# Optimization experiments

Hardware: AMD Instinct MI355X
Metric: run time of the kernel (lower is better)

## Reference

```python
import jax, jax.numpy as jnp
import numpy as np

N, E = 50000, 500000
IN_C, HID, OUT_C, HEADS, NL = 128, 16, 16, 8, 4
EPS = 1e-5
NEG_SLOPE = 0.2


def _gatv2(x, src, dst, Wl, Wr, att, bias, concat):
    # GATv2Conv (PyG semantics, eval mode): lin_l on source, lin_r on target,
    # e = a . LeakyReLU(xl[src] + xr[dst]); segment softmax over dst; scatter-sum.
    n = x.shape[0]
    H, C = att.shape
    xl = (x @ Wl).reshape(n, H, C)
    xr = (x @ Wr).reshape(n, H, C)
    e = jax.nn.leaky_relu(xl[src] + xr[dst], NEG_SLOPE)          # [E', H, C]
    logit = jnp.einsum('ehc,hc->eh', e, att)                      # [E', H]
    mx = jax.lax.stop_gradient(jax.ops.segment_max(logit, dst, num_segments=n))
    a = jnp.exp(logit - mx[dst])
    denom = jax.ops.segment_sum(a, dst, num_segments=n)
    alpha = a / denom[dst]                                        # [E', H]
    out = jax.ops.segment_sum(xl[src] * alpha[..., None], dst, num_segments=n)
    out = out.reshape(n, H * C) if concat else out.mean(axis=1)
    return out + bias


def _bn_eval(x, g, b, m, v):
    return (x - m) * jax.lax.rsqrt(v + EPS) * g + b


def setup_inputs() -> dict:
    key = jax.random.key(0)
    ks = jax.random.split(key, 32)
    d = {}
    d['x'] = jax.random.normal(ks[0], (N, IN_C), dtype=jnp.float32)
    d['edge_index'] = jax.random.randint(ks[1], (2, E), 0, N, dtype=jnp.int64)
    HC = HID * HEADS  # 128
    dims_in = [IN_C, HC, HC, HC]
    dims_h = [HEADS, HEADS, HEADS, 1]
    dims_c = [HID, HID, HID, OUT_C]
    ki = 2
    for i in range(NL):
        fan = dims_in[i]
        s = 1.0 / np.sqrt(fan)
        d[f'W{i}l'] = jax.random.uniform(ks[ki], (fan, dims_h[i] * dims_c[i]), minval=-s, maxval=s, dtype=jnp.float32); ki += 1
        d[f'W{i}r'] = jax.random.uniform(ks[ki], (fan, dims_h[i] * dims_c[i]), minval=-s, maxval=s, dtype=jnp.float32); ki += 1
        d[f'a{i}'] = jax.random.normal(ks[ki], (dims_h[i], dims_c[i]), dtype=jnp.float32) * 0.1; ki += 1
        out_dim = dims_h[i] * dims_c[i] if i < NL - 1 else dims_c[i]
        d[f'b{i}'] = jnp.zeros((out_dim,), dtype=jnp.float32)
    for i in range(NL - 1):
        d[f'g{i}'] = jnp.ones((HC,), dtype=jnp.float32) + 0.1 * jax.random.normal(ks[ki], (HC,), dtype=jnp.float32); ki += 1
        d[f'be{i}'] = 0.1 * jax.random.normal(ks[ki], (HC,), dtype=jnp.float32); ki += 1
        d[f'm{i}'] = 0.1 * jax.random.normal(ks[ki], (HC,), dtype=jnp.float32); ki += 1
        d[f'v{i}'] = jnp.ones((HC,), dtype=jnp.float32)
    return d


def reference(x, edge_index, W0l, W0r, a0, b0, W1l, W1r, a1, b1, W2l, W2r, a2, b2, W3l, W3r, a3, b3, g0, be0, m0, v0, g1, be1, m1, v1, g2, be2, m2, v2):
    n = x.shape[0]
    loop = jnp.arange(n, dtype=edge_index.dtype)
    src = jnp.concatenate([edge_index[0], loop])  # add_self_loops=True (PyG default)
    dst = jnp.concatenate([edge_index[1], loop])
    Ws = [(W0l, W0r, a0, b0), (W1l, W1r, a1, b1), (W2l, W2r, a2, b2), (W3l, W3r, a3, b3)]
    bns = [(g0, be0, m0, v0), (g1, be1, m1, v1), (g2, be2, m2, v2)]
    h = x
    for i in range(NL):
        Wl, Wr, att, bias = Ws[i]
        h = _gatv2(h, src, dst, Wl, Wr, att, bias, concat=(i < NL - 1))
        if i < NL - 1:
            g, b, m, v = bns[i]
            h = jax.nn.elu(_bn_eval(h, g, b, m, v))
    return h
```

## Files before the change

### kernel.cpp

```cpp
#include <hip/hip_runtime.h>
#include <hip/hip_fp16.h>
#include <math.h>

static constexpr float BN_EPS = 1e-5f;
static constexpr float NEG = 0.2f;

typedef float f32x4 __attribute__((ext_vector_type(4)));
typedef _Float16 h16x2 __attribute__((ext_vector_type(2)));
typedef _Float16 h16x8 __attribute__((ext_vector_type(8)));


__global__ __launch_bounds__(256) void hist_pack(
    const int* __restrict__ ei, int E, int n, int* __restrict__ cnt,
    const float* __restrict__ W0l, const float* __restrict__ W0r,
    const float* __restrict__ W1l, const float* __restrict__ W1r,
    const float* __restrict__ W2l, const float* __restrict__ W2r,
    const float* __restrict__ W3l, const float* __restrict__ W3r,
    __half* __restrict__ pk0, __half* __restrict__ pk1,
    __half* __restrict__ pk2, __half* __restrict__ pk3) {
    int b = blockIdx.x;
    if (b < 200) {
        if (threadIdx.x >= 64) return;
        const float *Wl, *Wr;
        __half* packed;
        int tile, NTT, M;
        if (b < 192) {
            int layer = b >> 6;
            tile = b & 63;
            NTT = 16; M = 128;
            Wl = (layer == 0) ? W0l : (layer == 1) ? W1l : W2l;
            Wr = (layer == 0) ? W0r : (layer == 1) ? W1r : W2r;
            packed = (layer == 0) ? pk0 : (layer == 1) ? pk1 : pk2;
        } else {
            tile = b - 192;
            NTT = 2; M = 16;
            Wl = W3l; Wr = W3r; packed = pk3;
        }
        int NT = NTT >> 1;
        int gnt = tile % NTT;
        int kt = tile / NTT;
        int l = threadIdx.x;
        const float* W = (gnt < NT) ? Wl : Wr;
        int col = (gnt % NT) * 16 + (l & 15);
        int krow = kt * 32 + ((l >> 4) << 3);
        size_t base = (size_t)tile * 512 + (size_t)l * 8;
#pragma unroll
        for (int j = 0; j < 8; j++)
            packed[base + j] = __float2half(W[(size_t)(krow + j) * M + col]);
    } else {
        int e = (b - 200) * 256 + threadIdx.x;
        int ET = E + n;
        if (e >= ET) return;
        int d = (e < E) ? ei[E + e] : (e - E);
        atomicAdd(&cnt[d], 1);
    }
}


__global__ void scan_block(const int* __restrict__ cnt, int* __restrict__ rowptr,
                           int* __restrict__ bsums, int n) {
    __shared__ int s[1024];
    int i = blockIdx.x * 1024 + threadIdx.x;
    int vv = (i < n) ? cnt[i] : 0;
    s[threadIdx.x] = vv;
    __syncthreads();
    for (int d = 1; d < 1024; d <<= 1) {
        int t = (threadIdx.x >= d) ? s[threadIdx.x - d] : 0;
        __syncthreads();
        s[threadIdx.x] += t;
        __syncthreads();
    }
    if (i < n) rowptr[i + 1] = s[threadIdx.x];
    if (threadIdx.x == 1023) bsums[blockIdx.x] = s[1023];
}

__global__ void scan_bsums(int* __restrict__ bsums, int nb) {
    int L = threadIdx.x;
    int v = (L < nb) ? bsums[L] : 0;
    for (int d = 1; d < 64; d <<= 1) {
        int t = __shfl_up(v, d);
        if (L >= d) v += t;
    }
    int ex = __shfl_up(v, 1);
    if (L == 0) ex = 0;
    if (L < nb) bsums[L] = ex;
}

__global__ void scan_add(int* __restrict__ rowptr, const int* __restrict__ bsums, int n) {
    int i = blockIdx.x * 1024 + threadIdx.x;
    if (i < n) rowptr[i + 1] += bsums[blockIdx.x];
    if (i == 0) rowptr[0] = 0;
}

__global__ void scatter_kernel(const int* __restrict__ ei, int E, int n,
                               const int* __restrict__ rowptr, int* __restrict__ fill,
                               int* __restrict__ col) {
    int e = blockIdx.x * blockDim.x + threadIdx.x;
    int ET = E + n;
    if (e >= ET) return;
    int s, d;
    if (e < E) { s = ei[e]; d = ei[E + e]; } else { s = e - E; d = s; }
    int pos = atomicAdd(&fill[d], 1);
    col[rowptr[d] + pos] = s;
}


template <bool FIRST>
__global__ __launch_bounds__(256) void gemm_h_big(
    const __half* __restrict__ xh, const float* __restrict__ xf,
    const __half* __restrict__ packed,
    __half* __restrict__ Y1, __half* __restrict__ Y2, int n) {
    __shared__ _Float16 sA[64 * 136];
    const int t = threadIdx.x;
    const int row0 = blockIdx.x * 64;

    for (int c = t; c < 1024; c += 256) {
        int row = c >> 4;
        int off = (c & 15) * 8;
        int gr = row0 + row;
        if (gr >= n) gr = n - 1;
        if (FIRST) {
            float4 v0 = *(const float4*)&xf[(size_t)gr * 128 + off];
            float4 v1 = *(const float4*)&xf[(size_t)gr * 128 + off + 4];
            h16x8 h = {(_Float16)v0.x, (_Float16)v0.y, (_Float16)v0.z, (_Float16)v0.w,
                       (_Float16)v1.x, (_Float16)v1.y, (_Float16)v1.z, (_Float16)v1.w};
            *(h16x8*)&sA[row * 136 + off] = h;
        } else {
            *(h16x8*)&sA[row * 136 + off] = *(const h16x8*)&xh[(size_t)gr * 128 + off];
        }
    }
    __syncthreads();

    const int lane = t & 63;
    const int s = t >> 6;
    const int lr = lane & 15;
    const int kq = (lane >> 4) * 8;

    h16x8 af[4][4];
#pragma unroll
    for (int rt = 0; rt < 4; rt++)
#pragma unroll
        for (int kt = 0; kt < 4; kt++)
            af[rt][kt] = *(const h16x8*)&sA[(rt * 16 + lr) * 136 + kt * 32 + kq];

    f32x4 acc[4][4];
#pragma unroll
    for (int a = 0; a < 4; a++)
#pragma unroll
        for (int b = 0; b < 4; b++) acc[a][b] = (f32x4){0.f, 0.f, 0.f, 0.f};

#pragma unroll
    for (int kt = 0; kt < 4; kt++) {
#pragma unroll
        for (int ntl = 0; ntl < 4; ntl++) {
            int nt = s * 4 + ntl;
            h16x8 b = *(const h16x8*)&packed[((size_t)(kt * 16 + nt)) * 512 + lane * 8];
#pragma unroll
            for (int rt = 0; rt < 4; rt++)
                acc[ntl][rt] = __builtin_amdgcn_mfma_f32_16x16x32_f16(af[rt][kt], b, acc[ntl][rt], 0, 0, 0);
        }
    }

    __half* Y = (s < 2) ? Y1 : Y2;
    const int colh = (s & 1) * 64;
    const int rq = (lane >> 4) * 4;
#pragma unroll
    for (int ntl = 0; ntl < 4; ntl++) {
        int col = colh + ntl * 16 + lr;
#pragma unroll
        for (int rt = 0; rt < 4; rt++) {
#pragma unroll
            for (int g = 0; g < 4; g++) {
                int row = row0 + rt * 16 + rq + g;
                if (row < n) Y[(size_t)row * 128 + col] = __float2half(acc[ntl][rt][g]);
            }
        }
    }
}


__global__ __launch_bounds__(256) void gemm_h_small(
    const __half* __restrict__ xh, const __half* __restrict__ packed,
    float* __restrict__ Y1, float* __restrict__ Y2, int n) {
    int lane = threadIdx.x & 63;
    int wv = blockIdx.x * 4 + (threadIdx.x >> 6);
    int row0 = wv * 16;
    if (row0 >= n) return;
    int r = row0 + (lane & 15);
    if (r >= n) r = n - 1;
    int kq = (lane >> 4) * 8;

    h16x8 af[4];
#pragma unroll
    for (int kt = 0; kt < 4; kt++)
        af[kt] = *(const h16x8*)&xh[(size_t)r * 128 + kt * 32 + kq];

    f32x4 acc[2];
    acc[0] = (f32x4){0.f, 0.f, 0.f, 0.f};
    acc[1] = (f32x4){0.f, 0.f, 0.f, 0.f};

#pragma unroll
    for (int kt = 0; kt < 4; kt++) {
#pragma unroll
        for (int nt = 0; nt < 2; nt++) {
            h16x8 b = *(const h16x8*)&packed[((size_t)(kt * 2 + nt)) * 512 + lane * 8];
            acc[nt] = __builtin_amdgcn_mfma_f32_16x16x32_f16(af[kt], b, acc[nt], 0, 0, 0);
        }
    }

    int colb = lane & 15;
    int rbase = row0 + (lane >> 4) * 4;
#pragma unroll
    for (int nt = 0; nt < 2; nt++) {
        float* Y = (nt == 0) ? Y1 : Y2;
#pragma unroll
        for (int g = 0; g < 4; g++) {
            int row = rbase + g;
            if (row < n) Y[(size_t)row * 16 + colb] = acc[nt][g];
        }
    }
}


__device__ __forceinline__ float dot4_h(h16x2 l01, h16x2 l23,
                                        h16x2 a01, h16x2 a23) {
#if __has_builtin(__builtin_amdgcn_fdot2)
    float part = __builtin_amdgcn_fdot2(l01, a01, 0.f, false);
    return __builtin_amdgcn_fdot2(l23, a23, part, false);
#else
    return fmaf((float)l01.x, (float)a01.x, fmaf((float)l01.y, (float)a01.y,
           fmaf((float)l23.x, (float)a23.x, (float)l23.y * (float)a23.y)));
#endif
}

__global__ __launch_bounds__(256) void agg_h(
    const __half* __restrict__ xl, const __half* __restrict__ xr,
    const int* __restrict__ rowptr, const int* __restrict__ col,
    const float* __restrict__ att, const float* __restrict__ bias,
    const float* __restrict__ g, const float* __restrict__ be,
    const float* __restrict__ bm, const float* __restrict__ bv,
    __half* __restrict__ oh, int n) {
    int v = (blockIdx.x * blockDim.x + threadIdx.x) >> 6;
    if (v >= n) return;
    int lane = threadIdx.x & 63;
    int half = lane >> 5;
    int L = lane & 31;
    int ch = 4 * L;

    float2 rraw = *(const float2*)&xr[(size_t)v * 128 + ch];
    h16x2 rx01 = *(h16x2*)&rraw.x;
    h16x2 rx23 = *(h16x2*)&rraw.y;
    float4 av = *(const float4*)&att[ch];
    h16x2 a01 = {(_Float16)av.x, (_Float16)av.y};
    h16x2 a23 = {(_Float16)av.z, (_Float16)av.w};
    const h16x2 neg2 = {(_Float16)NEG, (_Float16)NEG};

    int beg = rowptr[v];
    int end = rowptr[v + 1];

    float lrun = 0.f;
    float4 acc = make_float4(0.f, 0.f, 0.f, 0.f);

    auto proc = [&](float2 raw, bool ok) {
        h16x2 h01 = *(h16x2*)&raw.x;
        h16x2 h23 = *(h16x2*)&raw.y;
        h16x2 s01 = h01 + rx01;
        h16x2 s23 = h23 + rx23;
        h16x2 l01 = __builtin_elementwise_max(s01, s01 * neg2);
        h16x2 l23 = __builtin_elementwise_max(s23, s23 * neg2);
        float part = dot4_h(l01, l23, a01, a23);
        part += __shfl_xor(part, 1);
        part += __shfl_xor(part, 2);
        float p = ok ? __expf(part) : 0.f;
        lrun += p;
        acc.x = fmaf(p, (float)h01.x, acc.x);
        acc.y = fmaf(p, (float)h01.y, acc.y);
        acc.z = fmaf(p, (float)h23.x, acc.z);
        acc.w = fmaf(p, (float)h23.y, acc.w);
    };

    int e = beg;
    for (; e + 8 <= end; e += 8) {
        float2 r[4];
#pragma unroll
        for (int j = 0; j < 4; j++) {
            int u = col[e + 2 * j + half];
            r[j] = *(const float2*)&xl[((size_t)u << 7) + ch];
        }
#pragma unroll
        for (int j = 0; j < 4; j++) proc(r[j], true);
    }
    for (; e < end; e += 4) {
        float2 r[2];
        bool ok[2];
#pragma unroll
        for (int j = 0; j < 2; j++) {
            int idx = e + 2 * j + half;
            ok[j] = (idx < end);
            r[j] = make_float2(0.f, 0.f);
            if (ok[j]) {
                int u = col[idx];
                r[j] = *(const float2*)&xl[((size_t)u << 7) + ch];
            }
        }
#pragma unroll
        for (int j = 0; j < 2; j++) proc(r[j], ok[j]);
    }

    lrun += __shfl_xor(lrun, 32);
    acc.x += __shfl_xor(acc.x, 32);
    acc.y += __shfl_xor(acc.y, 32);
    acc.z += __shfl_xor(acc.z, 32);
    acc.w += __shfl_xor(acc.w, 32);

    if (half == 0) {
        float inv = 1.0f / lrun;
        float4 b4 = *(const float4*)&bias[ch];
        float o[4] = {fmaf(acc.x, inv, b4.x), fmaf(acc.y, inv, b4.y),
                      fmaf(acc.z, inv, b4.z), fmaf(acc.w, inv, b4.w)};
        float4 m4 = *(const float4*)&bm[ch];
        float4 v4 = *(const float4*)&bv[ch];
        float4 g4 = *(const float4*)&g[ch];
        float4 e4 = *(const float4*)&be[ch];
        float ms[4] = {m4.x, m4.y, m4.z, m4.w};
        float vs[4] = {v4.x, v4.y, v4.z, v4.w};
        float gs[4] = {g4.x, g4.y, g4.z, g4.w};
        float es[4] = {e4.x, e4.y, e4.z, e4.w};
        unsigned short h[4];
#pragma unroll
        for (int j = 0; j < 4; j++) {
            o[j] = (o[j] - ms[j]) * rsqrtf(vs[j] + BN_EPS) * gs[j] + es[j];
            o[j] = o[j] > 0.f ? o[j] : expm1f(o[j]);
            h[j] = __half_as_ushort(__float2half(o[j]));
        }
        *(ushort4*)&oh[(size_t)v * 128 + ch] = make_ushort4(h[0], h[1], h[2], h[3]);
    }
}


__global__ __launch_bounds__(256) void agg_f(
    const float* __restrict__ xl, const float* __restrict__ xr,
    const int* __restrict__ rowptr, const int* __restrict__ col,
    const float* __restrict__ att, const float* __restrict__ bias,
    float* __restrict__ out, int n) {
    int v = (blockIdx.x * blockDim.x + threadIdx.x) >> 6;
    if (v >= n) return;
    int lane = threadIdx.x & 63;
    int slot = lane >> 2;
    int L = lane & 3;
    int ch = 4 * L;

    float4 xrv = *(const float4*)&xr[(size_t)v * 16 + ch];
    float4 av = *(const float4*)&att[ch];
    int beg = rowptr[v];
    int end = rowptr[v + 1];

    float lrun = 0.f;
    float4 acc = make_float4(0.f, 0.f, 0.f, 0.f);

    for (int eb = beg; eb < end; eb += 16) {
        int idx = eb + slot;
        bool ok = (idx < end);
        float4 xv = make_float4(0.f, 0.f, 0.f, 0.f);
        if (ok) {
            int u = col[idx];
            xv = *(const float4*)&xl[((size_t)u << 4) + ch];
        }
        float s0 = xv.x + xrv.x; s0 = s0 > 0.f ? s0 : NEG * s0;
        float s1 = xv.y + xrv.y; s1 = s1 > 0.f ? s1 : NEG * s1;
        float s2 = xv.z + xrv.z; s2 = s2 > 0.f ? s2 : NEG * s2;
        float s3 = xv.w + xrv.w; s3 = s3 > 0.f ? s3 : NEG * s3;
        float part = fmaf(s0, av.x, fmaf(s1, av.y, fmaf(s2, av.z, s3 * av.w)));
        part += __shfl_xor(part, 1);
        part += __shfl_xor(part, 2);
        float p = ok ? __expf(part) : 0.f;
        lrun += p;
        acc.x = fmaf(p, xv.x, acc.x);
        acc.y = fmaf(p, xv.y, acc.y);
        acc.z = fmaf(p, xv.z, acc.z);
        acc.w = fmaf(p, xv.w, acc.w);
    }

#pragma unroll
    for (int d = 4; d < 64; d <<= 1) {
        lrun += __shfl_xor(lrun, d);
        acc.x += __shfl_xor(acc.x, d);
        acc.y += __shfl_xor(acc.y, d);
        acc.z += __shfl_xor(acc.z, d);
        acc.w += __shfl_xor(acc.w, d);
    }

    if (slot == 0) {
        float inv = 1.0f / lrun;
        float4 b4 = *(const float4*)&bias[ch];
        *(float4*)&out[(size_t)v * 16 + ch] =
            make_float4(fmaf(acc.x, inv, b4.x), fmaf(acc.y, inv, b4.y),
                        fmaf(acc.z, inv, b4.z), fmaf(acc.w, inv, b4.w));
    }
}


extern "C" void kernel_launch(void* const* d_in, const int* in_sizes, int n_in,
                              void* d_out, int out_size, void* d_ws, size_t ws_size,
                              hipStream_t stream) {
    const float* x = (const float*)d_in[0];
    const int* ei = (const int*)d_in[1];
    const float* Wl[4] = {(const float*)d_in[2], (const float*)d_in[6],
                          (const float*)d_in[10], (const float*)d_in[14]};
    const float* Wr[4] = {(const float*)d_in[3], (const float*)d_in[7],
                          (const float*)d_in[11], (const float*)d_in[15]};
    const float* att[4] = {(const float*)d_in[4], (const float*)d_in[8],
                           (const float*)d_in[12], (const float*)d_in[16]};
    const float* bias[4] = {(const float*)d_in[5], (const float*)d_in[9],
                            (const float*)d_in[13], (const float*)d_in[17]};
    const float* g[3] = {(const float*)d_in[18], (const float*)d_in[22], (const float*)d_in[26]};
    const float* be[3] = {(const float*)d_in[19], (const float*)d_in[23], (const float*)d_in[27]};
    const float* bm[3] = {(const float*)d_in[20], (const float*)d_in[24], (const float*)d_in[28]};
    const float* bv[3] = {(const float*)d_in[21], (const float*)d_in[25], (const float*)d_in[29]};

    const int n = in_sizes[0] / 128;
    const int E = in_sizes[1] / 2;
    const int ET = E + n;

    char* p = (char*)d_ws;
    __half* xh = (__half*)p;           p += (size_t)n * 128 * 2;
    __half* xlh = (__half*)p;          p += (size_t)n * 128 * 2;
    __half* xrh = (__half*)p;          p += (size_t)n * 128 * 2;
    float* xl3 = (float*)p;            p += (size_t)n * 16 * 4;
    float* xr3 = (float*)p;            p += (size_t)n * 16 * 4;
    int* rowptr = (int*)p;            p += (size_t)(n + 1) * 4;
    int* cnt = (int*)p;               p += (size_t)n * 4;
    int* fill = (int*)p;              p += (size_t)n * 4;
    int* col = (int*)p;               p += (size_t)ET * 4;
    int* bsums = (int*)p;             p += 256;
    __half* pk[4];
    for (int i = 0; i < 3; i++) { pk[i] = (__half*)p; p += 4 * 16 * 512 * 2; }
    pk[3] = (__half*)p;               p += 4 * 2 * 512 * 2;

    (void)hipMemsetAsync(cnt, 0, (size_t)n * 8, stream);

    const int tb = 256;
    const int histBlocks = (ET + tb - 1) / tb;
    hist_pack<<<200 + histBlocks, tb, 0, stream>>>(
        ei, E, n, cnt,
        Wl[0], Wr[0], Wl[1], Wr[1], Wl[2], Wr[2], Wl[3], Wr[3],
        pk[0], pk[1], pk[2], pk[3]);
    int nb = (n + 1023) / 1024;
    scan_block<<<nb, 1024, 0, stream>>>(cnt, rowptr, bsums, n);
    scan_bsums<<<1, 64, 0, stream>>>(bsums, nb);
    scan_add<<<nb, 1024, 0, stream>>>(rowptr, bsums, n);
    scatter_kernel<<<(ET + tb - 1) / tb, tb, 0, stream>>>(ei, E, n, rowptr, fill, col);

    const int gb64 = (n + 63) / 64;
    const int gemmBlocksSmall = ((n + 15) / 16 + 3) / 4;
    const int aggBlocks = (n + 3) / 4;

    gemm_h_big<true><<<gb64, 256, 0, stream>>>(nullptr, x, pk[0], xlh, xrh, n);
    agg_h<<<aggBlocks, 256, 0, stream>>>(
        xlh, xrh, rowptr, col, att[0], bias[0], g[0], be[0], bm[0], bv[0], xh, n);
    for (int i = 1; i < 3; i++) {
        gemm_h_big<false><<<gb64, 256, 0, stream>>>(xh, nullptr, pk[i], xlh, xrh, n);
        agg_h<<<aggBlocks, 256, 0, stream>>>(
            xlh, xrh, rowptr, col, att[i], bias[i], g[i], be[i], bm[i], bv[i], xh, n);
    }
    gemm_h_small<<<gemmBlocksSmall, 256, 0, stream>>>(xh, pk[3], xl3, xr3, n);
    agg_f<<<aggBlocks, 256, 0, stream>>>(
        xl3, xr3, rowptr, col, att[3], bias[3], (float*)d_out, n);
}
```

Baseline: 363.6 us.

## Fuse scan with first GEMM, merge scan kernels, widen aggregation to 8-channel lanes

The block scan now runs in the same launch as the layer-0 GEMM, and the bsums scan is folded into the scan-add kernel, removing two launches. The half-precision aggregation is reorganised so each lane handles 8 channels with 16-byte loads and processes 4 edges per wave step. Neighbour indices are loaded once per 64-edge chunk and broadcast with shuffles instead of re-read per edge. The float aggregation uses the same shuffle-broadcast of indices. The cost is more registers per lane and added shuffle traffic.

```diff
diff --git a/kernel.cpp b/kernel.cpp
--- a/kernel.cpp
+++ b/kernel.cpp
@@ -57,38 +57,56 @@
 }
 
 
-__global__ void scan_block(const int* __restrict__ cnt, int* __restrict__ rowptr,
-                           int* __restrict__ bsums, int n) {
-    __shared__ int s[1024];
+__device__ __forceinline__ void scan_block_body256(
+    const int* __restrict__ cnt, int* __restrict__ rowptr,
+    int* __restrict__ bsums, int n, int bid, int* s) {
+    int t = threadIdx.x;
+    int base = bid * 1024 + t * 4;
+    int v0 = 0, v1 = 0, v2 = 0, v3 = 0;
+    if (base + 3 < n) {
+        v0 = cnt[base];     v1 = cnt[base + 1];
+        v2 = cnt[base + 2]; v3 = cnt[base + 3];
+    } else {
+        if (base < n)     v0 = cnt[base];
+        if (base + 1 < n) v1 = cnt[base + 1];
+        if (base + 2 < n) v2 = cnt[base + 2];
+        if (base + 3 < n) v3 = cnt[base + 3];
+    }
+    int p1 = v0 + v1, p2 = p1 + v2, p3 = p2 + v3;
+    s[t] = p3;
+    __syncthreads();
+    for (int d = 1; d < 256; d <<= 1) {
+        int tt = (t >= d) ? s[t - d] : 0;
+        __syncthreads();
+        s[t] += tt;
+        __syncthreads();
+    }
+    int ex = s[t] - p3;
+    if (base < n)     rowptr[base + 1] = ex + v0;
+    if (base + 1 < n) rowptr[base + 2] = ex + p1;
+    if (base + 2 < n) rowptr[base + 3] = ex + p2;
+    if (base + 3 < n) rowptr[base + 4] = ex + p3;
+    if (t == 255) bsums[bid] = s[255];
+}
+
+__global__ __launch_bounds__(1024) void scan_add2(
+    int* __restrict__ rowptr, const int* __restrict__ bsums, int n, int nb) {
+    __shared__ int sex;
+    if (threadIdx.x < 64) {
+        int L = threadIdx.x;
+        int v = (L < nb) ? bsums[L] : 0;
+#pragma unroll
+        for (int d = 1; d < 64; d <<= 1) {
+            int t = __shfl_up(v, d);
+            if (L >= d) v += t;
+        }
+        int ex = __shfl_up(v, 1);
+        if (L == 0) ex = 0;
+        if (L == (int)blockIdx.x) sex = ex;
+    }
+    __syncthreads();
     int i = blockIdx.x * 1024 + threadIdx.x;
-    int vv = (i < n) ? cnt[i] : 0;
-    s[threadIdx.x] = vv;
-    __syncthreads();
-    for (int d = 1; d < 1024; d <<= 1) {
-        int t = (threadIdx.x >= d) ? s[threadIdx.x - d] : 0;
-        __syncthreads();
-        s[threadIdx.x] += t;
-        __syncthreads();
-    }
-    if (i < n) rowptr[i + 1] = s[threadIdx.x];
-    if (threadIdx.x == 1023) bsums[blockIdx.x] = s[1023];
-}
-
-__global__ void scan_bsums(int* __restrict__ bsums, int nb) {
-    int L = threadIdx.x;
-    int v = (L < nb) ? bsums[L] : 0;
-    for (int d = 1; d < 64; d <<= 1) {
-        int t = __shfl_up(v, d);
-        if (L >= d) v += t;
-    }
-    int ex = __shfl_up(v, 1);
-    if (L == 0) ex = 0;
-    if (L < nb) bsums[L] = ex;
-}
-
-__global__ void scan_add(int* __restrict__ rowptr, const int* __restrict__ bsums, int n) {
-    int i = blockIdx.x * 1024 + threadIdx.x;
-    if (i < n) rowptr[i + 1] += bsums[blockIdx.x];
+    if (i < n) rowptr[i + 1] += sex;
     if (i == 0) rowptr[0] = 0;
 }
 
@@ -106,13 +124,13 @@
 
 
 template <bool FIRST>
-__global__ __launch_bounds__(256) void gemm_h_big(
+__device__ __forceinline__ void gemm_body(
     const __half* __restrict__ xh, const float* __restrict__ xf,
     const __half* __restrict__ packed,
-    __half* __restrict__ Y1, __half* __restrict__ Y2, int n) {
-    __shared__ _Float16 sA[64 * 136];
+    __half* __restrict__ Y1, __half* __restrict__ Y2, int n, int bid,
+    _Float16* sA) {
     const int t = threadIdx.x;
-    const int row0 = blockIdx.x * 64;
+    const int row0 = bid * 64;
 
     for (int c = t; c < 1024; c += 256) {
         int row = c >> 4;
@@ -178,6 +196,28 @@
     }
 }
 
+__global__ __launch_bounds__(256) void gemm_h_big2(
+    const __half* __restrict__ xh, const __half* __restrict__ packed,
+    __half* __restrict__ Y1, __half* __restrict__ Y2, int n) {
+    __shared__ __align__(16) char smem[64 * 136 * 2];
+    gemm_body<false>(xh, nullptr, packed, Y1, Y2, n, blockIdx.x, (_Float16*)smem);
+}
+
+__global__ __launch_bounds__(256) void scanblk_gemm0(
+    const int* __restrict__ cnt, int* __restrict__ rowptr,
+    int* __restrict__ bsums, int n, int nscan,
+    const float* __restrict__ xf, const __half* __restrict__ packed,
+    __half* __restrict__ Y1, __half* __restrict__ Y2) {
+    __shared__ __align__(16) char smem[64 * 136 * 2];
+    int b = blockIdx.x;
+    if (b < nscan) {
+        scan_block_body256(cnt, rowptr, bsums, n, b, (int*)smem);
+    } else {
+        gemm_body<true>(nullptr, xf, packed, Y1, Y2, n, b - nscan,
+                        (_Float16*)smem);
+    }
+}
+
 
 __global__ __launch_bounds__(256) void gemm_h_small(
     const __half* __restrict__ xh, const __half* __restrict__ packed,
@@ -222,14 +262,18 @@
 }
 
 
-__device__ __forceinline__ float dot4_h(h16x2 l01, h16x2 l23,
-                                        h16x2 a01, h16x2 a23) {
+__device__ __forceinline__ float dot8_h(const h16x2* lp, const h16x2* ap) {
 #if __has_builtin(__builtin_amdgcn_fdot2)
-    float part = __builtin_amdgcn_fdot2(l01, a01, 0.f, false);
-    return __builtin_amdgcn_fdot2(l23, a23, part, false);
+    float part = __builtin_amdgcn_fdot2(lp[0], ap[0], 0.f, false);
+    part = __builtin_amdgcn_fdot2(lp[1], ap[1], part, false);
+    part = __builtin_amdgcn_fdot2(lp[2], ap[2], part, false);
+    return __builtin_amdgcn_fdot2(lp[3], ap[3], part, false);
 #else
-    return fmaf((float)l01.x, (float)a01.x, fmaf((float)l01.y, (float)a01.y,
-           fmaf((float)l23.x, (float)a23.x, (float)l23.y * (float)a23.y)));
+    float part = 0.f;
+#pragma unroll
+    for (int i = 0; i < 4; i++)
+        part += (float)lp[i].x * (float)ap[i].x + (float)lp[i].y * (float)ap[i].y;
+    return part;
 #endif
 }
 
@@ -243,97 +287,94 @@
     int v = (blockIdx.x * blockDim.x + threadIdx.x) >> 6;
     if (v >= n) return;
     int lane = threadIdx.x & 63;
-    int half = lane >> 5;
-    int L = lane & 31;
-    int ch = 4 * L;
-
-    float2 rraw = *(const float2*)&xr[(size_t)v * 128 + ch];
-    h16x2 rx01 = *(h16x2*)&rraw.x;
-    h16x2 rx23 = *(h16x2*)&rraw.y;
-    float4 av = *(const float4*)&att[ch];
-    h16x2 a01 = {(_Float16)av.x, (_Float16)av.y};
-    h16x2 a23 = {(_Float16)av.z, (_Float16)av.w};
-    const h16x2 neg2 = {(_Float16)NEG, (_Float16)NEG};
+    int grp = lane >> 4;
+    int L = lane & 15;
+    int ch = L * 8;
+
+    h16x8 rx = *(const h16x8*)&xr[((size_t)v << 7) + ch];
+    float4 av0 = *(const float4*)&att[ch];
+    float4 av1 = *(const float4*)&att[ch + 4];
+    h16x2 a[4] = {{(_Float16)av0.x, (_Float16)av0.y},
+                  {(_Float16)av0.z, (_Float16)av0.w},
+                  {(_Float16)av1.x, (_Float16)av1.y},
+                  {(_Float16)av1.z, (_Float16)av1.w}};
+    const h16x8 neg8 = {(_Float16)NEG, (_Float16)NEG, (_Float16)NEG, (_Float16)NEG,
+                        (_Float16)NEG, (_Float16)NEG, (_Float16)NEG, (_Float16)NEG};
 
     int beg = rowptr[v];
     int end = rowptr[v + 1];
 
     float lrun = 0.f;
-    float4 acc = make_float4(0.f, 0.f, 0.f, 0.f);
-
-    auto proc = [&](float2 raw, bool ok) {
-        h16x2 h01 = *(h16x2*)&raw.x;
-        h16x2 h23 = *(h16x2*)&raw.y;
-        h16x2 s01 = h01 + rx01;
-        h16x2 s23 = h23 + rx23;
-        h16x2 l01 = __builtin_elementwise_max(s01, s01 * neg2);
-        h16x2 l23 = __builtin_elementwise_max(s23, s23 * neg2);
-        float part = dot4_h(l01, l23, a01, a23);
+    float acc[8] = {0.f, 0.f, 0.f, 0.f, 0.f, 0.f, 0.f, 0.f};
+
+    auto proc = [&](h16x8 hv, bool ok) {
+        h16x8 s = hv + rx;
+        h16x8 l = __builtin_elementwise_max(s, s * neg8);
+        const h16x2* lp = (const h16x2*)&l;
+        float part = dot8_h(lp, a);
         part += __shfl_xor(part, 1);
-        part += __shfl_xor(part, 2);
         float p = ok ? __expf(part) : 0.f;
         lrun += p;
-        acc.x = fmaf(p, (float)h01.x, acc.x);
-        acc.y = fmaf(p, (float)h01.y, acc.y);
-        acc.z = fmaf(p, (float)h23.x, acc.z);
-        acc.w = fmaf(p, (float)h23.y, acc.w);
+        const _Float16* hp = (const _Float16*)&hv;
+#pragma unroll
+        for (int k = 0; k < 8; k++) acc[k] = fmaf(p, (float)hp[k], acc[k]);
     };
 
-    int e = beg;
-    for (; e + 8 <= end; e += 8) {
-        float2 r[4];
-#pragma unroll
-        for (int j = 0; j < 4; j++) {
-            int u = col[e + 2 * j + half];
-            r[j] = *(const float2*)&xl[((size_t)u << 7) + ch];
-        }
-#pragma unroll
-        for (int j = 0; j < 4; j++) proc(r[j], true);
-    }
-    for (; e < end; e += 4) {
-        float2 r[2];
-        bool ok[2];
-#pragma unroll
-        for (int j = 0; j < 2; j++) {
-            int idx = e + 2 * j + half;
-            ok[j] = (idx < end);
-            r[j] = make_float2(0.f, 0.f);
-            if (ok[j]) {
-                int u = col[idx];
-                r[j] = *(const float2*)&xl[((size_t)u << 7) + ch];
-            }
-        }
-#pragma unroll
-        for (int j = 0; j < 2; j++) proc(r[j], ok[j]);
-    }
-
+    for (int cb = beg; cb < end; cb += 64) {
+        int ce = min(end, cb + 64);
+        int cidx = (cb + lane < end) ? col[cb + lane] : v;
+        int e = cb;
+        for (; e + 8 <= ce; e += 8) {
+            int u0 = __shfl(cidx, e - cb + grp);
+            int u1 = __shfl(cidx, e - cb + 4 + grp);
+            h16x8 h0 = *(const h16x8*)&xl[((size_t)u0 << 7) + ch];
+            h16x8 h1 = *(const h16x8*)&xl[((size_t)u1 << 7) + ch];
+            proc(h0, true);
+            proc(h1, true);
+        }
+        for (; e < ce; e += 4) {
+            bool ok = (e + grp < ce);
+            int u = __shfl(cidx, e - cb + grp);
+            if (!ok) u = v;
+            h16x8 h0 = *(const h16x8*)&xl[((size_t)u << 7) + ch];
+            proc(h0, ok);
+        }
+    }
+
+    lrun += __shfl_xor(lrun, 16);
     lrun += __shfl_xor(lrun, 32);
-    acc.x += __shfl_xor(acc.x, 32);
-    acc.y += __shfl_xor(acc.y, 32);
-    acc.z += __shfl_xor(acc.z, 32);
-    acc.w += __shfl_xor(acc.w, 32);
-
-    if (half == 0) {
+#pragma unroll
+    for (int k = 0; k < 8; k++) {
+        acc[k] += __shfl_xor(acc[k], 16);
+        acc[k] += __shfl_xor(acc[k], 32);
+    }
+
+    if (grp == 0) {
         float inv = 1.0f / lrun;
-        float4 b4 = *(const float4*)&bias[ch];
-        float o[4] = {fmaf(acc.x, inv, b4.x), fmaf(acc.y, inv, b4.y),
-                      fmaf(acc.z, inv, b4.z), fmaf(acc.w, inv, b4.w)};
-        float4 m4 = *(const float4*)&bm[ch];
-        float4 v4 = *(const float4*)&bv[ch];
-        float4 g4 = *(const float4*)&g[ch];
-        float4 e4 = *(const float4*)&be[ch];
-        float ms[4] = {m4.x, m4.y, m4.z, m4.w};
-        float vs[4] = {v4.x, v4.y, v4.z, v4.w};
-        float gs[4] = {g4.x, g4.y, g4.z, g4.w};
-        float es[4] = {e4.x, e4.y, e4.z, e4.w};
-        unsigned short h[4];
-#pragma unroll
-        for (int j = 0; j < 4; j++) {
-            o[j] = (o[j] - ms[j]) * rsqrtf(vs[j] + BN_EPS) * gs[j] + es[j];
-            o[j] = o[j] > 0.f ? o[j] : expm1f(o[j]);
-            h[j] = __half_as_ushort(__float2half(o[j]));
-        }
-        *(ushort4*)&oh[(size_t)v * 128 + ch] = make_ushort4(h[0], h[1], h[2], h[3]);
+        float4 b0 = *(const float4*)&bias[ch];
+        float4 b1 = *(const float4*)&bias[ch + 4];
+        float4 m0 = *(const float4*)&bm[ch];
+        float4 m1 = *(const float4*)&bm[ch + 4];
+        float4 v0 = *(const float4*)&bv[ch];
+        float4 v1 = *(const float4*)&bv[ch + 4];
+        float4 g0 = *(const float4*)&g[ch];
+        float4 g1 = *(const float4*)&g[ch + 4];
+        float4 e0 = *(const float4*)&be[ch];
+        float4 e1 = *(const float4*)&be[ch + 4];
+        float bb[8] = {b0.x, b0.y, b0.z, b0.w, b1.x, b1.y, b1.z, b1.w};
+        float ms[8] = {m0.x, m0.y, m0.z, m0.w, m1.x, m1.y, m1.z, m1.w};
+        float vs[8] = {v0.x, v0.y, v0.z, v0.w, v1.x, v1.y, v1.z, v1.w};
+        float gs[8] = {g0.x, g0.y, g0.z, g0.w, g1.x, g1.y, g1.z, g1.w};
+        float es[8] = {e0.x, e0.y, e0.z, e0.w, e1.x, e1.y, e1.z, e1.w};
+        h16x8 outv;
+#pragma unroll
+        for (int k = 0; k < 8; k++) {
+            float o = fmaf(acc[k], inv, bb[k]);
+            o = (o - ms[k]) * rsqrtf(vs[k] + BN_EPS) * gs[k] + es[k];
+            o = o > 0.f ? o : expm1f(o);
+            outv[k] = (_Float16)o;
+        }
+        *(h16x8*)&oh[((size_t)v << 7) + ch] = outv;
     }
 }
 
@@ -350,7 +391,7 @@
     int L = lane & 3;
     int ch = 4 * L;
 
-    float4 xrv = *(const float4*)&xr[(size_t)v * 16 + ch];
+    float4 xrv = *(const float4*)&xr[((size_t)v << 4) + ch];
     float4 av = *(const float4*)&att[ch];
     int beg = rowptr[v];
     int end = rowptr[v + 1];
@@ -358,27 +399,28 @@
     float lrun = 0.f;
     float4 acc = make_float4(0.f, 0.f, 0.f, 0.f);
 
-    for (int eb = beg; eb < end; eb += 16) {
-        int idx = eb + slot;
-        bool ok = (idx < end);
-        float4 xv = make_float4(0.f, 0.f, 0.f, 0.f);
-        if (ok) {
-            int u = col[idx];
-            xv = *(const float4*)&xl[((size_t)u << 4) + ch];
-        }
-        float s0 = xv.x + xrv.x; s0 = s0 > 0.f ? s0 : NEG * s0;
-        float s1 = xv.y + xrv.y; s1 = s1 > 0.f ? s1 : NEG * s1;
-        float s2 = xv.z + xrv.z; s2 = s2 > 0.f ? s2 : NEG * s2;
-        float s3 = xv.w + xrv.w; s3 = s3 > 0.f ? s3 : NEG * s3;
-        float part = fmaf(s0, av.x, fmaf(s1, av.y, fmaf(s2, av.z, s3 * av.w)));
-        part += __shfl_xor(part, 1);
-        part += __shfl_xor(part, 2);
-        float p = ok ? __expf(part) : 0.f;
-        lrun += p;
-        acc.x = fmaf(p, xv.x, acc.x);
-        acc.y = fmaf(p, xv.y, acc.y);
-        acc.z = fmaf(p, xv.z, acc.z);
-        acc.w = fmaf(p, xv.w, acc.w);
+    for (int cb = beg; cb < end; cb += 64) {
+        int ce = min(end, cb + 64);
+        int cidx = (cb + lane < end) ? col[cb + lane] : v;
+        for (int e = cb; e < ce; e += 16) {
+            bool ok = (e + slot < ce);
+            int u = __shfl(cidx, e - cb + slot);
+            if (!ok) u = v;
+            float4 xv = *(const float4*)&xl[((size_t)u << 4) + ch];
+            float s0 = xv.x + xrv.x; s0 = s0 > 0.f ? s0 : NEG * s0;
+            float s1 = xv.y + xrv.y; s1 = s1 > 0.f ? s1 : NEG * s1;
+            float s2 = xv.z + xrv.z; s2 = s2 > 0.f ? s2 : NEG * s2;
+            float s3 = xv.w + xrv.w; s3 = s3 > 0.f ? s3 : NEG * s3;
+            float part = fmaf(s0, av.x, fmaf(s1, av.y, fmaf(s2, av.z, s3 * av.w)));
+            part += __shfl_xor(part, 1);
+            part += __shfl_xor(part, 2);
+            float p = ok ? __expf(part) : 0.f;
+            lrun += p;
+            acc.x = fmaf(p, xv.x, acc.x);
+            acc.y = fmaf(p, xv.y, acc.y);
+            acc.z = fmaf(p, xv.z, acc.z);
+            acc.w = fmaf(p, xv.w, acc.w);
+        }
     }
 
 #pragma unroll
@@ -393,7 +435,7 @@
     if (slot == 0) {
         float inv = 1.0f / lrun;
         float4 b4 = *(const float4*)&bias[ch];
-        *(float4*)&out[(size_t)v * 16 + ch] =
+        *(float4*)&out[((size_t)v << 4) + ch] =
             make_float4(fmaf(acc.x, inv, b4.x), fmaf(acc.y, inv, b4.y),
                         fmaf(acc.z, inv, b4.z), fmaf(acc.w, inv, b4.w));
     }
@@ -428,7 +470,7 @@
     __half* xrh = (__half*)p;          p += (size_t)n * 128 * 2;
     float* xl3 = (float*)p;            p += (size_t)n * 16 * 4;
     float* xr3 = (float*)p;            p += (size_t)n * 16 * 4;
-    int* rowptr = (int*)p;            p += (size_t)(n + 1) * 4;
+    int* rowptr = (int*)p;            p += (size_t)(n + 4) * 4;
     int* cnt = (int*)p;               p += (size_t)n * 4;
     int* fill = (int*)p;              p += (size_t)n * 4;
     int* col = (int*)p;               p += (size_t)ET * 4;
@@ -445,21 +487,21 @@
         ei, E, n, cnt,
         Wl[0], Wr[0], Wl[1], Wr[1], Wl[2], Wr[2], Wl[3], Wr[3],
         pk[0], pk[1], pk[2], pk[3]);
-    int nb = (n + 1023) / 1024;
-    scan_block<<<nb, 1024, 0, stream>>>(cnt, rowptr, bsums, n);
-    scan_bsums<<<1, 64, 0, stream>>>(bsums, nb);
-    scan_add<<<nb, 1024, 0, stream>>>(rowptr, bsums, n);
-    scatter_kernel<<<(ET + tb - 1) / tb, tb, 0, stream>>>(ei, E, n, rowptr, fill, col);
-
+
+    const int nb = (n + 1023) / 1024;
     const int gb64 = (n + 63) / 64;
     const int gemmBlocksSmall = ((n + 15) / 16 + 3) / 4;
     const int aggBlocks = (n + 3) / 4;
 
-    gemm_h_big<true><<<gb64, 256, 0, stream>>>(nullptr, x, pk[0], xlh, xrh, n);
+    scanblk_gemm0<<<nb + gb64, 256, 0, stream>>>(
+        cnt, rowptr, bsums, n, nb, x, pk[0], xlh, xrh);
+    scan_add2<<<nb, 1024, 0, stream>>>(rowptr, bsums, n, nb);
+    scatter_kernel<<<(ET + tb - 1) / tb, tb, 0, stream>>>(ei, E, n, rowptr, fill, col);
+
     agg_h<<<aggBlocks, 256, 0, stream>>>(
         xlh, xrh, rowptr, col, att[0], bias[0], g[0], be[0], bm[0], bv[0], xh, n);
     for (int i = 1; i < 3; i++) {
-        gemm_h_big<false><<<gb64, 256, 0, stream>>>(xh, nullptr, pk[i], xlh, xrh, n);
+        gemm_h_big2<<<gb64, 256, 0, stream>>>(xh, pk[i], xlh, xrh, n);
         agg_h<<<aggBlocks, 256, 0, stream>>>(
             xlh, xrh, rowptr, col, att[i], bias[i], g[i], be[i], bm[i], bv[i], xh, n);
     }
```

After: 375.4 us. +3.3%, slower.
